# Performance work log

Measured on AMD Instinct MI355X. Metric: run time of the kernel, lower is better.

## Reference

```python
import jax, jax.numpy as jnp
import numpy as np

N = 200_000   # mesh nodes
C = 400_000   # cells (~2N for triangular mesh)
K = 3 * C     # cells_node / cells_index flat length (3 nodes per cell)
E = 600_000   # cell-cell edges (faces)
D = 128       # feature dim
H = 128       # MLP hidden


def setup_inputs() -> dict:
    key = jax.random.key(0)
    ks = jax.random.split(key, 6)
    node_attr = jax.random.normal(ks[0], (N, D), dtype=jnp.float32)
    edge_attr = jax.random.normal(ks[1], (E, D), dtype=jnp.float32)
    W1 = jax.random.normal(ks[2], (3 * D, H), dtype=jnp.float32) * 0.05
    b1 = jnp.zeros((H,), dtype=jnp.float32)
    W2 = jax.random.normal(ks[3], (H, D), dtype=jnp.float32) * 0.05
    b2 = jnp.zeros((D,), dtype=jnp.float32)
    cells_node = jax.random.randint(ks[4], (K,), 0, N, dtype=jnp.int32)
    # each cell owns 3 consecutive node slots (faithful FVM incidence structure)
    cells_index = jnp.repeat(jnp.arange(C, dtype=jnp.int32), 3)
    edge_index = jax.random.randint(ks[5], (2, E), 0, C, dtype=jnp.int32)
    return dict(node_attr=node_attr, edge_attr=edge_attr, W1=W1, b1=b1,
                W2=W2, b2=b2, cells_node=cells_node, cells_index=cells_index,
                edge_index=edge_index)


def reference(node_attr, edge_attr, W1, b1, W2, b2,
              cells_node, cells_index, edge_index):
    # node -> cell scatter-sum (calc_cell_centered_with_node_attr, map=True)
    gathered = node_attr[cells_node]                      # [K, D]
    cell_attr = jax.ops.segment_sum(gathered, cells_index, num_segments=C)  # [C, D]
    senders, receivers = edge_index[0], edge_index[1]
    mask = (senders != receivers)[:, None].astype(node_attr.dtype)  # [E, 1]
    senders_attr = cell_attr[senders]                     # [E, D]
    receivers_attr = cell_attr[receivers] * mask          # zero self-edges
    collected = jnp.concatenate([senders_attr, receivers_attr, edge_attr], axis=1)  # [E, 3D]
    h = jax.nn.relu(collected @ W1 + b1)                  # [E, H]
    edge_attr_new = h @ W2 + b2                           # [E, D]
    return edge_attr_new
```

## Files before the change

### kernel.cpp

```cpp
#include <hip/hip_runtime.h>

typedef short bf16x8 __attribute__((ext_vector_type(8)));
typedef float f32x4 __attribute__((ext_vector_type(4)));

#define MAX_C 400000
#define MAX_E 600000

__device__ __align__(16) unsigned short g_W1t[128 * 384];
__device__ __align__(16) unsigned short g_W2t[128 * 128];
__device__ __align__(16) unsigned short g_cell[((size_t)MAX_C + 1) * 128];
__device__ __align__(16) unsigned short g_edge[(size_t)MAX_E * 128];

__device__ __forceinline__ unsigned short f2bf(float f) {
    union { unsigned int i; float f; } v; v.f = f;
    return (unsigned short)((v.i + 0x7FFFu + ((v.i >> 16) & 1u)) >> 16);
}

__global__ __launch_bounds__(256) void prep_kernel(
        const float* __restrict__ node_attr,
        const float* __restrict__ edge_attr,
        const int* __restrict__ cells_node,
        int C, int E, int cellBlocks)
{
    int t = threadIdx.x;
    if ((int)blockIdx.x < cellBlocks) {
        int grp = blockIdx.x * 16 + (t >> 4);
        int sub = t & 15;
        int c0 = grp * 2, c1 = c0 + 1;
        if (c0 >= C || c0 >= MAX_C) return;
        int ja[3], jb[3];
        ja[0] = cells_node[c0 * 3 + 0];
        ja[1] = cells_node[c0 * 3 + 1];
        ja[2] = cells_node[c0 * 3 + 2];
        bool d1 = (c1 < C) && (c1 < MAX_C);
        jb[0] = d1 ? cells_node[c1 * 3 + 0] : ja[0];
        jb[1] = d1 ? cells_node[c1 * 3 + 1] : ja[1];
        jb[2] = d1 ? cells_node[c1 * 3 + 2] : ja[2];

        float a0[8] = {0.f,0.f,0.f,0.f,0.f,0.f,0.f,0.f};
        float a1[8] = {0.f,0.f,0.f,0.f,0.f,0.f,0.f,0.f};
        #pragma unroll
        for (int j = 0; j < 3; ++j) {
            const float* p = node_attr + (size_t)ja[j] * 128 + sub * 8;
            float4 v0 = *(const float4*)(p);
            float4 v1 = *(const float4*)(p + 4);
            a0[0] += v0.x; a0[1] += v0.y; a0[2] += v0.z; a0[3] += v0.w;
            a0[4] += v1.x; a0[5] += v1.y; a0[6] += v1.z; a0[7] += v1.w;
        }
        #pragma unroll
        for (int j = 0; j < 3; ++j) {
            const float* p = node_attr + (size_t)jb[j] * 128 + sub * 8;
            float4 v0 = *(const float4*)(p);
            float4 v1 = *(const float4*)(p + 4);
            a1[0] += v0.x; a1[1] += v0.y; a1[2] += v0.z; a1[3] += v0.w;
            a1[4] += v1.x; a1[5] += v1.y; a1[6] += v1.z; a1[7] += v1.w;
        }
        uint4 o0, o1;
        o0.x = (unsigned)f2bf(a0[0]) | ((unsigned)f2bf(a0[1]) << 16);
        o0.y = (unsigned)f2bf(a0[2]) | ((unsigned)f2bf(a0[3]) << 16);
        o0.z = (unsigned)f2bf(a0[4]) | ((unsigned)f2bf(a0[5]) << 16);
        o0.w = (unsigned)f2bf(a0[6]) | ((unsigned)f2bf(a0[7]) << 16);
        *(uint4*)(g_cell + (size_t)c0 * 128 + sub * 8) = o0;
        if (d1) {
            o1.x = (unsigned)f2bf(a1[0]) | ((unsigned)f2bf(a1[1]) << 16);
            o1.y = (unsigned)f2bf(a1[2]) | ((unsigned)f2bf(a1[3]) << 16);
            o1.z = (unsigned)f2bf(a1[4]) | ((unsigned)f2bf(a1[5]) << 16);
            o1.w = (unsigned)f2bf(a1[6]) | ((unsigned)f2bf(a1[7]) << 16);
            *(uint4*)(g_cell + (size_t)c1 * 128 + sub * 8) = o1;
        }
    } else {
        long i = (long)((int)blockIdx.x - cellBlocks) * 256 + t;
        if (i >= (long)E * 16) return;
        const float* p = edge_attr + i * 8;
        float4 v0 = *(const float4*)(p);
        float4 v1 = *(const float4*)(p + 4);
        uint4 o;
        o.x = (unsigned)f2bf(v0.x) | ((unsigned)f2bf(v0.y) << 16);
        o.y = (unsigned)f2bf(v0.z) | ((unsigned)f2bf(v0.w) << 16);
        o.z = (unsigned)f2bf(v1.x) | ((unsigned)f2bf(v1.y) << 16);
        o.w = (unsigned)f2bf(v1.z) | ((unsigned)f2bf(v1.w) << 16);
        *(uint4*)(g_edge + i * 8) = o;
    }
}

__global__ __launch_bounds__(256) void wprep_kernel(
        const float* __restrict__ W1,
        const float* __restrict__ W2)
{
    int i = blockIdx.x * 256 + threadIdx.x;
    if (i < 384 * 128) {
        int n = i / 384, k = i % 384;
        g_W1t[i] = f2bf(W1[k * 128 + n]);
    } else {
        int j = i - 384 * 128;
        int n = j / 128, k = j % 128;
        g_W2t[j] = f2bf(W2[k * 128 + n]);
    }
}

__global__ __launch_bounds__(256) void edge_mlp_kernel(
        const float* __restrict__ b1,
        const float* __restrict__ b2,
        const int* __restrict__ senders,
        const int* __restrict__ receivers,
        float* __restrict__ out, int E)
{
    __shared__ __align__(16) unsigned short Hs[128][136];

    const int t  = threadIdx.x;
    const int e0 = blockIdx.x * 128;
    const int wv = t >> 6;
    const int l  = t & 63;
    const int lr = l & 15;
    const int q  = l >> 4;

    unsigned os[8], orr[8], oe[8];
    #pragma unroll
    for (int nt = 0; nt < 8; ++nt) {
        int e = e0 + nt * 16 + lr;
        if (e > E - 1) e = E - 1;
        int s = senders[e];
        int r = receivers[e];
        os[nt]  = (unsigned)s * 256u;
        orr[nt] = (s == r) ? (unsigned)MAX_C * 256u : (unsigned)r * 256u;
        oe[nt]  = (unsigned)e * 256u;
    }

    const unsigned qb  = (unsigned)(q * 16);
    const unsigned ow0 = (unsigned)((wv * 32 + lr) * 768) + qb;
    const unsigned ow1 = ow0 + 16u * 768u;

    const char* cellb = (const char*)g_cell;
    const char* edgeb = (const char*)g_edge;
    const char* w1b   = (const char*)g_W1t;
    const char* w2b   = (const char*)g_W2t;

    f32x4 acc[2][8];
    #pragma unroll
    for (int m = 0; m < 2; ++m)
        #pragma unroll
        for (int nt = 0; nt < 8; ++nt) acc[m][nt] = (f32x4)(0.f);

    bf16x8 aF[2][2], bF[2][8];

    auto l1load = [&](int kc, int p) {
        if (kc < 4) {
            #pragma unroll
            for (int nt = 0; nt < 8; ++nt)
                bF[p][nt] = *(const bf16x8*)(cellb + (size_t)(os[nt] + qb + kc * 64));
        } else if (kc < 8) {
            #pragma unroll
            for (int nt = 0; nt < 8; ++nt)
                bF[p][nt] = *(const bf16x8*)(cellb + (size_t)(orr[nt] + qb + (kc - 4) * 64));
        } else {
            #pragma unroll
            for (int nt = 0; nt < 8; ++nt)
                bF[p][nt] = *(const bf16x8*)(edgeb + (size_t)(oe[nt] + qb + (kc - 8) * 64));
        }
        aF[p][0] = *(const bf16x8*)(w1b + (size_t)(ow0 + kc * 64));
        aF[p][1] = *(const bf16x8*)(w1b + (size_t)(ow1 + kc * 64));
    };

    l1load(0, 0);
    #pragma unroll
    for (int kc = 0; kc < 12; ++kc) {
        const int cur = kc & 1;
        if (kc + 1 < 12) l1load(kc + 1, cur ^ 1);
        #pragma unroll
        for (int nt = 0; nt < 8; ++nt) {
            acc[0][nt] = __builtin_amdgcn_mfma_f32_16x16x32_bf16(aF[cur][0], bF[cur][nt], acc[0][nt], 0, 0, 0);
            acc[1][nt] = __builtin_amdgcn_mfma_f32_16x16x32_bf16(aF[cur][1], bF[cur][nt], acc[1][nt], 0, 0, 0);
        }
    }

    #pragma unroll
    for (int m = 0; m < 2; ++m) {
        const int hc = wv * 32 + m * 16 + q * 4;
        const float4 bv = *(const float4*)(b1 + hc);
        #pragma unroll
        for (int nt = 0; nt < 8; ++nt) {
            float v0 = acc[m][nt][0] + bv.x; v0 = v0 > 0.f ? v0 : 0.f;
            float v1 = acc[m][nt][1] + bv.y; v1 = v1 > 0.f ? v1 : 0.f;
            float v2 = acc[m][nt][2] + bv.z; v2 = v2 > 0.f ? v2 : 0.f;
            float v3 = acc[m][nt][3] + bv.w; v3 = v3 > 0.f ? v3 : 0.f;
            uint2 w;
            w.x = (unsigned)f2bf(v0) | ((unsigned)f2bf(v1) << 16);
            w.y = (unsigned)f2bf(v2) | ((unsigned)f2bf(v3) << 16);
            *(uint2*)&Hs[nt * 16 + lr][hc] = w;
        }
    }

    const unsigned ow20 = (unsigned)((wv * 32 + lr) * 256) + qb;
    const unsigned ow21 = ow20 + 16u * 256u;
    bf16x8 w2f[2][4];
    #pragma unroll
    for (int kc = 0; kc < 4; ++kc) {
        w2f[0][kc] = *(const bf16x8*)(w2b + (size_t)(ow20 + kc * 64));
        w2f[1][kc] = *(const bf16x8*)(w2b + (size_t)(ow21 + kc * 64));
    }
    __syncthreads();

    f32x4 acc2[2][8];
    #pragma unroll
    for (int m = 0; m < 2; ++m)
        #pragma unroll
        for (int nt = 0; nt < 8; ++nt) acc2[m][nt] = (f32x4)(0.f);

    #pragma unroll
    for (int kc = 0; kc < 4; ++kc) {
        #pragma unroll
        for (int nt = 0; nt < 8; ++nt) {
            bf16x8 b = *(const bf16x8*)&Hs[nt * 16 + lr][kc * 32 + q * 8];
            acc2[0][nt] = __builtin_amdgcn_mfma_f32_16x16x32_bf16(w2f[0][kc], b, acc2[0][nt], 0, 0, 0);
            acc2[1][nt] = __builtin_amdgcn_mfma_f32_16x16x32_bf16(w2f[1][kc], b, acc2[1][nt], 0, 0, 0);
        }
    }

    #pragma unroll
    for (int m = 0; m < 2; ++m) {
        const int oc = wv * 32 + m * 16 + q * 4;
        const float4 bv = *(const float4*)(b2 + oc);
        #pragma unroll
        for (int nt = 0; nt < 8; ++nt) {
            int e = e0 + nt * 16 + lr;
            if (e < E) {
                float4 v;
                v.x = acc2[m][nt][0] + bv.x;
                v.y = acc2[m][nt][1] + bv.y;
                v.z = acc2[m][nt][2] + bv.z;
                v.w = acc2[m][nt][3] + bv.w;
                *(float4*)(out + (size_t)e * 128 + oc) = v;
            }
        }
    }
}

extern "C" void kernel_launch(void* const* d_in, const int* in_sizes, int n_in,
                              void* d_out, int out_size, void* d_ws, size_t ws_size,
                              hipStream_t stream)
{
    const float* node_attr = (const float*)d_in[0];
    const float* edge_attr = (const float*)d_in[1];
    const float* W1 = (const float*)d_in[2];
    const float* b1 = (const float*)d_in[3];
    const float* W2 = (const float*)d_in[4];
    const float* b2 = (const float*)d_in[5];
    const int* cells_node  = (const int*)d_in[6];
    const int* edge_index  = (const int*)d_in[8];
    float* out = (float*)d_out;

    int E = in_sizes[1] / 128;
    int C = in_sizes[6] / 3;

    const int* senders = edge_index;
    const int* receivers = edge_index + E;

    int cellBlocks = (C + 31) / 32;
    int edgeBlocks = (int)(((long)E * 16 + 255) / 256);

    hipLaunchKernelGGL(prep_kernel, dim3(cellBlocks + edgeBlocks), dim3(256), 0, stream,
                       node_attr, edge_attr, cells_node, C, E, cellBlocks);
    hipLaunchKernelGGL(wprep_kernel, dim3((384 * 128 + 128 * 128) / 256), dim3(256), 0, stream,
                       W1, W2);
    hipLaunchKernelGGL(edge_mlp_kernel, dim3((E + 127) / 128), dim3(256), 0, stream,
                       b1, b2, senders, receivers, out, E);
}
```

Baseline: 1.035 ms.

## Fuse edge_attr bf16 conversion into MLP and repartition waves by edges

Drops the separate pass that converts edge_attr to a bf16 copy. The MLP kernel now reads fp32 edge_attr directly and converts it in registers, which removes a full write and re-read of the edge tensor. Each wave now owns 32 edges across all 128 output features instead of 32 features across all 128 edges. This lets the second GEMM read only the wave's own Hs rows and drop the __syncthreads, at the cost of every wave streaming the full W1/W2 from global/L2 each k-step. The cell gather also changes which 16-byte chunks each lane reads per node row.

```diff
diff --git a/kernel.cpp b/kernel.cpp
--- a/kernel.cpp
+++ b/kernel.cpp
@@ -4,82 +4,67 @@
 typedef float f32x4 __attribute__((ext_vector_type(4)));
 
 #define MAX_C 400000
-#define MAX_E 600000
 
 __device__ __align__(16) unsigned short g_W1t[128 * 384];
 __device__ __align__(16) unsigned short g_W2t[128 * 128];
 __device__ __align__(16) unsigned short g_cell[((size_t)MAX_C + 1) * 128];
-__device__ __align__(16) unsigned short g_edge[(size_t)MAX_E * 128];
 
 __device__ __forceinline__ unsigned short f2bf(float f) {
     union { unsigned int i; float f; } v; v.f = f;
     return (unsigned short)((v.i + 0x7FFFu + ((v.i >> 16) & 1u)) >> 16);
 }
 
-__global__ __launch_bounds__(256) void prep_kernel(
+__global__ __launch_bounds__(256) void cell_kernel(
         const float* __restrict__ node_attr,
-        const float* __restrict__ edge_attr,
-        const int* __restrict__ cells_node,
-        int C, int E, int cellBlocks)
+        const int* __restrict__ cells_node, int C)
 {
     int t = threadIdx.x;
-    if ((int)blockIdx.x < cellBlocks) {
-        int grp = blockIdx.x * 16 + (t >> 4);
-        int sub = t & 15;
-        int c0 = grp * 2, c1 = c0 + 1;
-        if (c0 >= C || c0 >= MAX_C) return;
-        int ja[3], jb[3];
-        ja[0] = cells_node[c0 * 3 + 0];
-        ja[1] = cells_node[c0 * 3 + 1];
-        ja[2] = cells_node[c0 * 3 + 2];
-        bool d1 = (c1 < C) && (c1 < MAX_C);
-        jb[0] = d1 ? cells_node[c1 * 3 + 0] : ja[0];
-        jb[1] = d1 ? cells_node[c1 * 3 + 1] : ja[1];
-        jb[2] = d1 ? cells_node[c1 * 3 + 2] : ja[2];
-
-        float a0[8] = {0.f,0.f,0.f,0.f,0.f,0.f,0.f,0.f};
-        float a1[8] = {0.f,0.f,0.f,0.f,0.f,0.f,0.f,0.f};
-        #pragma unroll
-        for (int j = 0; j < 3; ++j) {
-            const float* p = node_attr + (size_t)ja[j] * 128 + sub * 8;
-            float4 v0 = *(const float4*)(p);
-            float4 v1 = *(const float4*)(p + 4);
-            a0[0] += v0.x; a0[1] += v0.y; a0[2] += v0.z; a0[3] += v0.w;
-            a0[4] += v1.x; a0[5] += v1.y; a0[6] += v1.z; a0[7] += v1.w;
-        }
-        #pragma unroll
-        for (int j = 0; j < 3; ++j) {
-            const float* p = node_attr + (size_t)jb[j] * 128 + sub * 8;
-            float4 v0 = *(const float4*)(p);
-            float4 v1 = *(const float4*)(p + 4);
-            a1[0] += v0.x; a1[1] += v0.y; a1[2] += v0.z; a1[3] += v0.w;
-            a1[4] += v1.x; a1[5] += v1.y; a1[6] += v1.z; a1[7] += v1.w;
-        }
-        uint4 o0, o1;
-        o0.x = (unsigned)f2bf(a0[0]) | ((unsigned)f2bf(a0[1]) << 16);
-        o0.y = (unsigned)f2bf(a0[2]) | ((unsigned)f2bf(a0[3]) << 16);
-        o0.z = (unsigned)f2bf(a0[4]) | ((unsigned)f2bf(a0[5]) << 16);
-        o0.w = (unsigned)f2bf(a0[6]) | ((unsigned)f2bf(a0[7]) << 16);
-        *(uint4*)(g_cell + (size_t)c0 * 128 + sub * 8) = o0;
-        if (d1) {
-            o1.x = (unsigned)f2bf(a1[0]) | ((unsigned)f2bf(a1[1]) << 16);
-            o1.y = (unsigned)f2bf(a1[2]) | ((unsigned)f2bf(a1[3]) << 16);
-            o1.z = (unsigned)f2bf(a1[4]) | ((unsigned)f2bf(a1[5]) << 16);
-            o1.w = (unsigned)f2bf(a1[6]) | ((unsigned)f2bf(a1[7]) << 16);
-            *(uint4*)(g_cell + (size_t)c1 * 128 + sub * 8) = o1;
-        }
-    } else {
-        long i = (long)((int)blockIdx.x - cellBlocks) * 256 + t;
-        if (i >= (long)E * 16) return;
-        const float* p = edge_attr + i * 8;
-        float4 v0 = *(const float4*)(p);
-        float4 v1 = *(const float4*)(p + 4);
-        uint4 o;
-        o.x = (unsigned)f2bf(v0.x) | ((unsigned)f2bf(v0.y) << 16);
-        o.y = (unsigned)f2bf(v0.z) | ((unsigned)f2bf(v0.w) << 16);
-        o.z = (unsigned)f2bf(v1.x) | ((unsigned)f2bf(v1.y) << 16);
-        o.w = (unsigned)f2bf(v1.z) | ((unsigned)f2bf(v1.w) << 16);
-        *(uint4*)(g_edge + i * 8) = o;
+    int grp = blockIdx.x * 16 + (t >> 4);
+    int sub = t & 15;
+    int c0 = grp * 2, c1 = c0 + 1;
+    if (c0 >= C) return;
+    bool d1 = (c1 < C);
+
+    int ja[3], jb[3];
+    ja[0] = cells_node[c0 * 3 + 0];
+    ja[1] = cells_node[c0 * 3 + 1];
+    ja[2] = cells_node[c0 * 3 + 2];
+    jb[0] = d1 ? cells_node[c1 * 3 + 0] : ja[0];
+    jb[1] = d1 ? cells_node[c1 * 3 + 1] : ja[1];
+    jb[2] = d1 ? cells_node[c1 * 3 + 2] : ja[2];
+
+    float aL[4] = {0.f,0.f,0.f,0.f}, aH[4] = {0.f,0.f,0.f,0.f};
+    float bL[4] = {0.f,0.f,0.f,0.f}, bH[4] = {0.f,0.f,0.f,0.f};
+    #pragma unroll
+    for (int j = 0; j < 3; ++j) {
+        const float* r = node_attr + (size_t)ja[j] * 128;
+        float4 lo = *(const float4*)(r + sub * 4);
+        float4 hi = *(const float4*)(r + 64 + sub * 4);
+        aL[0] += lo.x; aL[1] += lo.y; aL[2] += lo.z; aL[3] += lo.w;
+        aH[0] += hi.x; aH[1] += hi.y; aH[2] += hi.z; aH[3] += hi.w;
+    }
+    #pragma unroll
+    for (int j = 0; j < 3; ++j) {
+        const float* r = node_attr + (size_t)jb[j] * 128;
+        float4 lo = *(const float4*)(r + sub * 4);
+        float4 hi = *(const float4*)(r + 64 + sub * 4);
+        bL[0] += lo.x; bL[1] += lo.y; bL[2] += lo.z; bL[3] += lo.w;
+        bH[0] += hi.x; bH[1] += hi.y; bH[2] += hi.z; bH[3] += hi.w;
+    }
+    uint2 o;
+    o.x = (unsigned)f2bf(aL[0]) | ((unsigned)f2bf(aL[1]) << 16);
+    o.y = (unsigned)f2bf(aL[2]) | ((unsigned)f2bf(aL[3]) << 16);
+    *(uint2*)(g_cell + (size_t)c0 * 128 + sub * 4) = o;
+    o.x = (unsigned)f2bf(aH[0]) | ((unsigned)f2bf(aH[1]) << 16);
+    o.y = (unsigned)f2bf(aH[2]) | ((unsigned)f2bf(aH[3]) << 16);
+    *(uint2*)(g_cell + (size_t)c0 * 128 + 64 + sub * 4) = o;
+    if (d1) {
+        o.x = (unsigned)f2bf(bL[0]) | ((unsigned)f2bf(bL[1]) << 16);
+        o.y = (unsigned)f2bf(bL[2]) | ((unsigned)f2bf(bL[3]) << 16);
+        *(uint2*)(g_cell + (size_t)c1 * 128 + sub * 4) = o;
+        o.x = (unsigned)f2bf(bH[0]) | ((unsigned)f2bf(bH[1]) << 16);
+        o.y = (unsigned)f2bf(bH[2]) | ((unsigned)f2bf(bH[3]) << 16);
+        *(uint2*)(g_cell + (size_t)c1 * 128 + 64 + sub * 4) = o;
     }
 }
 
@@ -99,6 +84,7 @@
 }
 
 __global__ __launch_bounds__(256) void edge_mlp_kernel(
+        const float* __restrict__ edge_attr,
         const float* __restrict__ b1,
         const float* __restrict__ b2,
         const int* __restrict__ senders,
@@ -108,128 +94,128 @@
     __shared__ __align__(16) unsigned short Hs[128][136];
 
     const int t  = threadIdx.x;
-    const int e0 = blockIdx.x * 128;
     const int wv = t >> 6;
     const int l  = t & 63;
     const int lr = l & 15;
     const int q  = l >> 4;
-
-    unsigned os[8], orr[8], oe[8];
-    #pragma unroll
-    for (int nt = 0; nt < 8; ++nt) {
-        int e = e0 + nt * 16 + lr;
+    const int e0 = blockIdx.x * 128;
+    const int eb = e0 + wv * 32;
+
+    unsigned os[2], orr[2]; int eidx[2];
+    #pragma unroll
+    for (int nt = 0; nt < 2; ++nt) {
+        int e = eb + nt * 16 + lr;
         if (e > E - 1) e = E - 1;
+        eidx[nt] = e;
         int s = senders[e];
         int r = receivers[e];
         os[nt]  = (unsigned)s * 256u;
         orr[nt] = (s == r) ? (unsigned)MAX_C * 256u : (unsigned)r * 256u;
-        oe[nt]  = (unsigned)e * 256u;
-    }
-
-    const unsigned qb  = (unsigned)(q * 16);
-    const unsigned ow0 = (unsigned)((wv * 32 + lr) * 768) + qb;
-    const unsigned ow1 = ow0 + 16u * 768u;
+    }
 
     const char* cellb = (const char*)g_cell;
-    const char* edgeb = (const char*)g_edge;
     const char* w1b   = (const char*)g_W1t;
     const char* w2b   = (const char*)g_W2t;
-
-    f32x4 acc[2][8];
-    #pragma unroll
-    for (int m = 0; m < 2; ++m)
-        #pragma unroll
-        for (int nt = 0; nt < 8; ++nt) acc[m][nt] = (f32x4)(0.f);
-
-    bf16x8 aF[2][2], bF[2][8];
-
-    auto l1load = [&](int kc, int p) {
+    const unsigned qb = (unsigned)(q * 16);
+
+    f32x4 acc[8][2];
+    #pragma unroll
+    for (int mt = 0; mt < 8; ++mt) { acc[mt][0] = (f32x4)(0.f); acc[mt][1] = (f32x4)(0.f); }
+
+    bf16x8 bB[3][2];
+    float4 rL[3][2], rH[3][2];
+
+    auto loadB = [&](int kc) {
+        int p = kc % 3;
         if (kc < 4) {
             #pragma unroll
-            for (int nt = 0; nt < 8; ++nt)
-                bF[p][nt] = *(const bf16x8*)(cellb + (size_t)(os[nt] + qb + kc * 64));
+            for (int nt = 0; nt < 2; ++nt)
+                bB[p][nt] = *(const bf16x8*)(cellb + (size_t)(os[nt] + qb + kc * 64));
         } else if (kc < 8) {
             #pragma unroll
-            for (int nt = 0; nt < 8; ++nt)
-                bF[p][nt] = *(const bf16x8*)(cellb + (size_t)(orr[nt] + qb + (kc - 4) * 64));
+            for (int nt = 0; nt < 2; ++nt)
+                bB[p][nt] = *(const bf16x8*)(cellb + (size_t)(orr[nt] + qb + (kc - 4) * 64));
         } else {
             #pragma unroll
-            for (int nt = 0; nt < 8; ++nt)
-                bF[p][nt] = *(const bf16x8*)(edgeb + (size_t)(oe[nt] + qb + (kc - 8) * 64));
-        }
-        aF[p][0] = *(const bf16x8*)(w1b + (size_t)(ow0 + kc * 64));
-        aF[p][1] = *(const bf16x8*)(w1b + (size_t)(ow1 + kc * 64));
+            for (int nt = 0; nt < 2; ++nt) {
+                const float* pp = edge_attr + (size_t)eidx[nt] * 128 + (kc - 8) * 32 + q * 8;
+                rL[p][nt] = *(const float4*)(pp);
+                rH[p][nt] = *(const float4*)(pp + 4);
+            }
+        }
     };
-
-    l1load(0, 0);
+    auto getB = [&](int kc, int nt) -> bf16x8 {
+        int p = kc % 3;
+        if (kc < 8) return bB[p][nt];
+        union { unsigned short u[8]; bf16x8 v; } r;
+        float4 lo = rL[p][nt], hi = rH[p][nt];
+        r.u[0] = f2bf(lo.x); r.u[1] = f2bf(lo.y); r.u[2] = f2bf(lo.z); r.u[3] = f2bf(lo.w);
+        r.u[4] = f2bf(hi.x); r.u[5] = f2bf(hi.y); r.u[6] = f2bf(hi.z); r.u[7] = f2bf(hi.w);
+        return r.v;
+    };
+
+    loadB(0); loadB(1);
     #pragma unroll
     for (int kc = 0; kc < 12; ++kc) {
-        const int cur = kc & 1;
-        if (kc + 1 < 12) l1load(kc + 1, cur ^ 1);
-        #pragma unroll
-        for (int nt = 0; nt < 8; ++nt) {
-            acc[0][nt] = __builtin_amdgcn_mfma_f32_16x16x32_bf16(aF[cur][0], bF[cur][nt], acc[0][nt], 0, 0, 0);
-            acc[1][nt] = __builtin_amdgcn_mfma_f32_16x16x32_bf16(aF[cur][1], bF[cur][nt], acc[1][nt], 0, 0, 0);
-        }
-    }
-
-    #pragma unroll
-    for (int m = 0; m < 2; ++m) {
-        const int hc = wv * 32 + m * 16 + q * 4;
-        const float4 bv = *(const float4*)(b1 + hc);
-        #pragma unroll
-        for (int nt = 0; nt < 8; ++nt) {
-            float v0 = acc[m][nt][0] + bv.x; v0 = v0 > 0.f ? v0 : 0.f;
-            float v1 = acc[m][nt][1] + bv.y; v1 = v1 > 0.f ? v1 : 0.f;
-            float v2 = acc[m][nt][2] + bv.z; v2 = v2 > 0.f ? v2 : 0.f;
-            float v3 = acc[m][nt][3] + bv.w; v3 = v3 > 0.f ? v3 : 0.f;
+        if (kc + 2 < 12) loadB(kc + 2);
+        bf16x8 bb0 = getB(kc, 0);
+        bf16x8 bb1 = getB(kc, 1);
+        #pragma unroll
+        for (int mt = 0; mt < 8; ++mt) {
+            bf16x8 a = *(const bf16x8*)(w1b + (size_t)((mt * 16 + lr) * 768 + kc * 64 + qb));
+            acc[mt][0] = __builtin_amdgcn_mfma_f32_16x16x32_bf16(a, bb0, acc[mt][0], 0, 0, 0);
+            acc[mt][1] = __builtin_amdgcn_mfma_f32_16x16x32_bf16(a, bb1, acc[mt][1], 0, 0, 0);
+        }
+    }
+
+    #pragma unroll
+    for (int mt = 0; mt < 8; ++mt) {
+        const int f = mt * 16 + q * 4;
+        const float4 bv = *(const float4*)(b1 + f);
+        #pragma unroll
+        for (int nt = 0; nt < 2; ++nt) {
+            int el = wv * 32 + nt * 16 + lr;
+            float v0 = acc[mt][nt][0] + bv.x; v0 = v0 > 0.f ? v0 : 0.f;
+            float v1 = acc[mt][nt][1] + bv.y; v1 = v1 > 0.f ? v1 : 0.f;
+            float v2 = acc[mt][nt][2] + bv.z; v2 = v2 > 0.f ? v2 : 0.f;
+            float v3 = acc[mt][nt][3] + bv.w; v3 = v3 > 0.f ? v3 : 0.f;
             uint2 w;
             w.x = (unsigned)f2bf(v0) | ((unsigned)f2bf(v1) << 16);
             w.y = (unsigned)f2bf(v2) | ((unsigned)f2bf(v3) << 16);
-            *(uint2*)&Hs[nt * 16 + lr][hc] = w;
-        }
-    }
-
-    const unsigned ow20 = (unsigned)((wv * 32 + lr) * 256) + qb;
-    const unsigned ow21 = ow20 + 16u * 256u;
-    bf16x8 w2f[2][4];
+            *(uint2*)&Hs[el][f] = w;
+        }
+    }
+
+    f32x4 acc2[8][2];
+    #pragma unroll
+    for (int mt = 0; mt < 8; ++mt) { acc2[mt][0] = (f32x4)(0.f); acc2[mt][1] = (f32x4)(0.f); }
+
     #pragma unroll
     for (int kc = 0; kc < 4; ++kc) {
-        w2f[0][kc] = *(const bf16x8*)(w2b + (size_t)(ow20 + kc * 64));
-        w2f[1][kc] = *(const bf16x8*)(w2b + (size_t)(ow21 + kc * 64));
-    }
-    __syncthreads();
-
-    f32x4 acc2[2][8];
-    #pragma unroll
-    for (int m = 0; m < 2; ++m)
-        #pragma unroll
-        for (int nt = 0; nt < 8; ++nt) acc2[m][nt] = (f32x4)(0.f);
-
-    #pragma unroll
-    for (int kc = 0; kc < 4; ++kc) {
-        #pragma unroll
-        for (int nt = 0; nt < 8; ++nt) {
-            bf16x8 b = *(const bf16x8*)&Hs[nt * 16 + lr][kc * 32 + q * 8];
-            acc2[0][nt] = __builtin_amdgcn_mfma_f32_16x16x32_bf16(w2f[0][kc], b, acc2[0][nt], 0, 0, 0);
-            acc2[1][nt] = __builtin_amdgcn_mfma_f32_16x16x32_bf16(w2f[1][kc], b, acc2[1][nt], 0, 0, 0);
-        }
-    }
-
-    #pragma unroll
-    for (int m = 0; m < 2; ++m) {
-        const int oc = wv * 32 + m * 16 + q * 4;
-        const float4 bv = *(const float4*)(b2 + oc);
-        #pragma unroll
-        for (int nt = 0; nt < 8; ++nt) {
-            int e = e0 + nt * 16 + lr;
+        bf16x8 h0 = *(const bf16x8*)&Hs[wv * 32 +      lr][kc * 32 + q * 8];
+        bf16x8 h1 = *(const bf16x8*)&Hs[wv * 32 + 16 + lr][kc * 32 + q * 8];
+        #pragma unroll
+        for (int mt = 0; mt < 8; ++mt) {
+            bf16x8 a = *(const bf16x8*)(w2b + (size_t)((mt * 16 + lr) * 256 + kc * 64 + qb));
+            acc2[mt][0] = __builtin_amdgcn_mfma_f32_16x16x32_bf16(a, h0, acc2[mt][0], 0, 0, 0);
+            acc2[mt][1] = __builtin_amdgcn_mfma_f32_16x16x32_bf16(a, h1, acc2[mt][1], 0, 0, 0);
+        }
+    }
+
+    #pragma unroll
+    for (int mt = 0; mt < 8; ++mt) {
+        const int f = mt * 16 + q * 4;
+        const float4 bv = *(const float4*)(b2 + f);
+        #pragma unroll
+        for (int nt = 0; nt < 2; ++nt) {
+            int e = eb + nt * 16 + lr;
             if (e < E) {
                 float4 v;
-                v.x = acc2[m][nt][0] + bv.x;
-                v.y = acc2[m][nt][1] + bv.y;
-                v.z = acc2[m][nt][2] + bv.z;
-                v.w = acc2[m][nt][3] + bv.w;
-                *(float4*)(out + (size_t)e * 128 + oc) = v;
+                v.x = acc2[mt][nt][0] + bv.x;
+                v.y = acc2[mt][nt][1] + bv.y;
+                v.z = acc2[mt][nt][2] + bv.z;
+                v.w = acc2[mt][nt][3] + bv.w;
+                *(float4*)(out + (size_t)e * 128 + f) = v;
             }
         }
     }
@@ -255,13 +241,9 @@
     const int* senders = edge_index;
     const int* receivers = edge_index + E;
 
-    int cellBlocks = (C + 31) / 32;
-    int edgeBlocks = (int)(((long)E * 16 + 255) / 256);
-
-    hipLaunchKernelGGL(prep_kernel, dim3(cellBlocks + edgeBlocks), dim3(256), 0, stream,
-                       node_attr, edge_attr, cells_node, C, E, cellBlocks);
-    hipLaunchKernelGGL(wprep_kernel, dim3((384 * 128 + 128 * 128) / 256), dim3(256), 0, stream,
-                       W1, W2);
+    hipLaunchKernelGGL(cell_kernel, dim3((C + 31) / 32), dim3(256), 0, stream,
+                       node_attr, cells_node, C);
+    hipLaunchKernelGGL(wprep_kernel, dim3(256), dim3(256), 0, stream, W1, W2);
     hipLaunchKernelGGL(edge_mlp_kernel, dim3((E + 127) / 128), dim3(256), 0, stream,
-                       b1, b2, senders, receivers, out, E);
-}
+                       edge_attr, b1, b2, senders, receivers, out, E);
+}
```

Result: faster. 1.004 ms (-2.9%).
